# Optimization experiments

Measured on AMD Instinct MI355X. Metric: run time of the kernel, lower is better.

## Reference

```python
import jax, jax.numpy as jnp
import numpy as np


def setup_inputs() -> dict:
    key = jax.random.key(0)
    kq, kk, kv = jax.random.split(key, 3)
    B, S, H, D = 1, 4096, 16, 64
    q = jax.random.normal(kq, (B, S, H, D), dtype=jnp.float32)
    k = jax.random.normal(kk, (B, S, H, D), dtype=jnp.float32)
    v = jax.random.normal(kv, (B, S, H, D), dtype=jnp.float32)
    return {"q": q, "k": k, "v": v, "causal": 1}


def reference(q, k, v, causal):
    B, S, H, D = q.shape
    scale = D ** (-0.5)
    # scores: [B, H, S_q, S_k]
    scores = jnp.einsum("bqhd,bkhd->bhqk", q, k) * scale
    if causal:
        mask = jnp.triu(jnp.ones((S, S), dtype=bool), k=1)  # True above diagonal
        scores = jnp.where(mask, -jnp.inf, scores)
    attn = jax.nn.softmax(scores, axis=-1)
    out = jnp.einsum("bhqk,bkhd->bqhd", attn, v)
    return out
```

## Files before the change

### kernel.cpp

```cpp
#include <hip/hip_runtime.h>
#include <stdint.h>

#define S_LEN 4096
#define NH    16
#define HD    64
#define RSTR  (NH * HD)
#define LRSTR 18

typedef __attribute__((ext_vector_type(8))) __bf16 bf16x8;
typedef __attribute__((ext_vector_type(4))) short short4v;
typedef __attribute__((ext_vector_type(4))) float floatx4;

union BF4 { unsigned short u[4]; unsigned d[2]; short4v s; };

__device__ __forceinline__ unsigned pkbf(float a, float b) {
    unsigned ua = __builtin_bit_cast(unsigned, a) + 0x8000u;
    unsigned ub = __builtin_bit_cast(unsigned, b) + 0x8000u;
    return __builtin_amdgcn_perm(ub, ua, 0x07060302u);
}

__device__ __forceinline__ floatx4 mfma16(short4v a, short4v b, floatx4 c) {
#if __has_builtin(__builtin_amdgcn_mfma_f32_16x16x16bf16_1k)
    return __builtin_amdgcn_mfma_f32_16x16x16bf16_1k(a, b, c, 0, 0, 0);
#else
    floatx4 d;
    asm volatile("v_mfma_f32_16x16x16_bf16 %0, %1, %2, %3\n\ts_nop 7\n\ts_nop 7"
                 : "=v"(d) : "v"(a), "v"(b), "v"(c));
    return d;
#endif
}

__device__ __forceinline__ void gl16(const void* g, void* l) {
#if __has_builtin(__builtin_amdgcn_global_load_lds)
    __builtin_amdgcn_global_load_lds((const __attribute__((address_space(1))) unsigned int*)g,
                                     (__attribute__((address_space(3))) unsigned int*)l, 16, 0, 0);
#else
    *(uint4*)l = *(const uint4*)g;
#endif
}

__global__ __launch_bounds__(256)
void pp_kv(const float* __restrict__ K, const float* __restrict__ V,
           unsigned short* __restrict__ Kz, unsigned short* __restrict__ Vz) {
    __shared__ __align__(16) float vt[64][68];
    const int bid = blockIdx.x;
    const int h   = bid & 15;
    const int tau = bid >> 4;
    const int tid = threadIdx.x;
    {
        const int r = tid >> 2, gg = tid & 3;
        const float* kp = K + ((size_t)(64 * tau + r) * NH + h) * HD + 16 * gg;
        const float4 a = *reinterpret_cast<const float4*>(kp);
        const float4 b = *reinterpret_cast<const float4*>(kp + 4);
        const float4 c = *reinterpret_cast<const float4*>(kp + 8);
        const float4 d = *reinterpret_cast<const float4*>(kp + 12);
        uint4 f0, f1;
        f0.x = pkbf(a.x, a.y); f0.y = pkbf(a.z, a.w);
        f0.z = pkbf(b.x, b.y); f0.w = pkbf(b.z, b.w);
        f1.x = pkbf(c.x, c.y); f1.y = pkbf(c.z, c.w);
        f1.z = pkbf(d.x, d.y); f1.w = pkbf(d.z, d.w);
        unsigned short* out = Kz + ((size_t)(h * 64 + tau)) * 4096 + r * 64;
        *reinterpret_cast<uint4*>(out + (((2 * gg)     ^ (r & 7)) * 8)) = f0;
        *reinterpret_cast<uint4*>(out + (((2 * gg + 1) ^ (r & 7)) * 8)) = f1;
    }
    {
        const int r = tid >> 2, ch = tid & 3;
        const float* vrow = V + ((size_t)(64 * tau + r) * NH + h) * HD + 4 * ch;
        #pragma unroll
        for (int k2 = 0; k2 < 4; ++k2)
            *reinterpret_cast<float4*>(&vt[r][4 * ch + 16 * k2]) =
                *reinterpret_cast<const float4*>(vrow + 16 * k2);
    }
    __syncthreads();
    {
        const int dr = tid & 63, kg = tid >> 6;
        float x[16];
        #pragma unroll
        for (int j = 0; j < 16; ++j) x[j] = vt[16 * kg + j][dr];
        uint4 g0, g1;
        g0.x = pkbf(x[0],  x[1]);  g0.y = pkbf(x[2],  x[3]);
        g0.z = pkbf(x[4],  x[5]);  g0.w = pkbf(x[6],  x[7]);
        g1.x = pkbf(x[8],  x[9]);  g1.y = pkbf(x[10], x[11]);
        g1.z = pkbf(x[12], x[13]); g1.w = pkbf(x[14], x[15]);
        unsigned short* out = Vz + ((size_t)(h * 64 + tau)) * 4096 + dr * 64;
        *reinterpret_cast<uint4*>(out + (((2 * kg)     ^ (dr & 7)) * 8)) = g0;
        *reinterpret_cast<uint4*>(out + (((2 * kg + 1) ^ (dr & 7)) * 8)) = g1;
    }
}

__global__ __launch_bounds__(256, 3)
void fa_main(const float* __restrict__ Q, const unsigned short* __restrict__ Kz,
             const unsigned short* __restrict__ Vz, const int* __restrict__ causal_p,
             float* __restrict__ O) {
    __shared__ __align__(16) unsigned char smem[49152];
    unsigned short* Klds = (unsigned short*)smem;
    unsigned short* Vlds = (unsigned short*)(smem + 24576);
    unsigned short* Qlds = (unsigned short*)(smem + 16384);
    float* Lsum = (float*)smem;
    float* Lred = (float*)(smem + 16384);

    const int bid = blockIdx.x;
    const int h   = bid & 15;
    const int x   = 63 - (bid >> 4);
    const int q0  = x * 64;

    const int tid = threadIdx.x;
    const int wv  = tid >> 6;
    const int ln  = tid & 63;
    const int c16 = ln & 15;
    const int qd  = ln >> 4;
    const int causal = causal_p[0];

    const float SC = 0.18033688011112042f;

    const char* kg = (const char*)Kz + (size_t)h * 64 * 8192 + wv * 2048 + ln * 16;
    const char* vg = (const char*)Vz + (size_t)h * 64 * 8192 + wv * 2048 + ln * 16;
    char* kl = (char*)smem + wv * 2048 + ln * 16;
    char* vl = (char*)smem + 24576 + wv * 2048 + ln * 16;

#define GLDS_TILE(IT, BUF) do {                                  \
    const char* ks_ = kg + (size_t)(IT) * 8192;                  \
    const char* vs_ = vg + (size_t)(IT) * 8192;                  \
    char* kd_ = kl + (BUF) * 8192;                               \
    char* vd_ = vl + (BUF) * 8192;                               \
    gl16(ks_, kd_); gl16(ks_ + 1024, kd_ + 1024);                \
    gl16(vs_, vd_); gl16(vs_ + 1024, vd_ + 1024);                \
} while (0)

    GLDS_TILE(0, 0);
    GLDS_TILE(1, 1);

    {
        const int r = tid >> 2, gg = tid & 3;
        const float* qp = Q + ((size_t)(q0 + r) * NH + h) * HD + 16 * gg;
        const float4 a = *reinterpret_cast<const float4*>(qp);
        const float4 b = *reinterpret_cast<const float4*>(qp + 4);
        const float4 c = *reinterpret_cast<const float4*>(qp + 8);
        const float4 d = *reinterpret_cast<const float4*>(qp + 12);
        uint4 f0, f1;
        f0.x = pkbf(a.x * SC, a.y * SC); f0.y = pkbf(a.z * SC, a.w * SC);
        f0.z = pkbf(b.x * SC, b.y * SC); f0.w = pkbf(b.z * SC, b.w * SC);
        f1.x = pkbf(c.x * SC, c.y * SC); f1.y = pkbf(c.z * SC, c.w * SC);
        f1.z = pkbf(d.x * SC, d.y * SC); f1.w = pkbf(d.z * SC, d.w * SC);
        unsigned short* out = Qlds + r * 64;
        *reinterpret_cast<uint4*>(out + (((2 * gg)     ^ (r & 7)) * 8)) = f0;
        *reinterpret_cast<uint4*>(out + (((2 * gg + 1) ^ (r & 7)) * 8)) = f1;
    }

    const int nIter = causal ? (x + 1) : (S_LEN / 64);

    floatx4 acc[4][4];
    #pragma unroll
    for (int m = 0; m < 4; ++m)
        #pragma unroll
        for (int t = 0; t < 4; ++t) acc[m][t] = floatx4{0.f, 0.f, 0.f, 0.f};
    float lacc[4] = {0.f, 0.f, 0.f, 0.f};

    const int e7 = c16 & 7;
    const int o0 = (qd ^ e7) * 8;
    const int o1 = ((4 + qd) ^ e7) * 8;
    const int vo = ((2 * wv + (qd >> 1)) ^ e7) * 8 + (qd & 1) * 4;
    const int mlhs = 16 * wv + 4 * qd;

    __syncthreads();

    bf16x8 qh0[4], qh1[4];
    #pragma unroll
    for (int t = 0; t < 4; ++t) {
        const unsigned short* qrow = Qlds + (16 * t + c16) * 64;
        qh0[t] = *reinterpret_cast<const bf16x8*>(qrow + o0);
        qh1[t] = *reinterpret_cast<const bf16x8*>(qrow + o1);
    }
    __syncthreads();

    int br = 0;
    int b2 = 2;
    for (int it = 0; it < nIter; ++it) {
        if (it == nIter - 1) {
            asm volatile("s_waitcnt vmcnt(0)" ::: "memory");
        } else {
            asm volatile("s_waitcnt vmcnt(4)" ::: "memory");
        }
        __builtin_amdgcn_s_barrier();

        if (it + 2 < nIter) GLDS_TILE(it + 2, b2);

        const unsigned short* Kb = Klds + br * 4096;
        const unsigned short* Vb = Vlds + br * 4096;

        const unsigned short* krow = Kb + (16 * wv + c16) * 64;
        const bf16x8 kf0 = *reinterpret_cast<const bf16x8*>(krow + o0);
        const bf16x8 kf1 = *reinterpret_cast<const bf16x8*>(krow + o1);

        const bool maskit = (causal != 0) && (it == nIter - 1);

        BF4 pf[4];
        #pragma unroll
        for (int t = 0; t < 4; ++t) {
            floatx4 st = __builtin_amdgcn_mfma_f32_16x16x32_bf16(
                kf0, qh0[t], floatx4{0.f, 0.f, 0.f, 0.f}, 0, 0, 0);
            st = __builtin_amdgcn_mfma_f32_16x16x32_bf16(kf1, qh1[t], st, 0, 0, 0);
            float p[4];
            #pragma unroll
            for (int i = 0; i < 4; ++i) {
                float sv = st[i];
                if (maskit && (mlhs + i > 16 * t + c16)) sv = -1e30f;
                p[i] = __builtin_amdgcn_exp2f(sv);
            }
            lacc[t] += (p[0] + p[1]) + (p[2] + p[3]);
            pf[t].d[0] = pkbf(p[0], p[1]);
            pf[t].d[1] = pkbf(p[2], p[3]);
        }

        #pragma unroll
        for (int md = 0; md < 4; ++md) {
            BF4 vf;
            const unsigned short* vrow = Vb + (16 * md + c16) * 64 + vo;
            *reinterpret_cast<uint2*>(&vf.d[0]) = *reinterpret_cast<const uint2*>(vrow);
            #pragma unroll
            for (int t = 0; t < 4; ++t)
                acc[md][t] = mfma16(vf.s, pf[t].s, acc[md][t]);
        }

        br = (br == 2) ? 0 : br + 1;
        b2 = (b2 == 2) ? 0 : b2 + 1;
    }

    __syncthreads();

    #pragma unroll
    for (int t = 0; t < 4; ++t) {
        float lt = lacc[t];
        lt += __shfl_xor(lt, 16);
        lt += __shfl_xor(lt, 32);
        if (qd == 0) Lsum[wv * 64 + t * 16 + c16] = lt;
    }

    const int qi  = tid & 63;
    const int dg  = tid >> 6;
    const int lnr = 16 * dg + (qi & 15);
    const int jb  = 4 * (qi >> 4);
    float* orow = O + ((size_t)(q0 + qi) * NH + h) * HD;
    float inv = 0.f;

    for (int md = 0; md < 4; ++md) {
        float* Lw = Lred + (wv * 64 + ln) * LRSTR;
        #pragma unroll
        for (int t = 0; t < 4; ++t) {
            float2 w0; w0.x = acc[md][t][0]; w0.y = acc[md][t][1];
            float2 w1; w1.x = acc[md][t][2]; w1.y = acc[md][t][3];
            *reinterpret_cast<float2*>(&Lw[4 * t])     = w0;
            *reinterpret_cast<float2*>(&Lw[4 * t + 2]) = w1;
        }
        __syncthreads();
        if (md == 0) {
            const float l = Lsum[qi] + Lsum[64 + qi] + Lsum[128 + qi] + Lsum[192 + qi];
            inv = 1.0f / l;
        }
        float s0 = 0.f, s1 = 0.f, s2 = 0.f, s3 = 0.f;
        #pragma unroll
        for (int w = 0; w < 4; ++w) {
            const float* Lr = Lred + (w * 64 + lnr) * LRSTR + jb;
            s0 += Lr[0]; s1 += Lr[1]; s2 += Lr[2]; s3 += Lr[3];
        }
        floatx4 o; o[0] = s0 * inv; o[1] = s1 * inv; o[2] = s2 * inv; o[3] = s3 * inv;
        *reinterpret_cast<floatx4*>(orow + 16 * md + 4 * dg) = o;
        __syncthreads();
    }
}

extern "C" void kernel_launch(void* const* d_in, const int* in_sizes, int n_in,
                              void* d_out, int out_size, void* d_ws, size_t ws_size,
                              hipStream_t stream) {
    const float* q = (const float*)d_in[0];
    const float* k = (const float*)d_in[1];
    const float* v = (const float*)d_in[2];
    const int* causal = (const int*)d_in[3];
    float* out = (float*)d_out;
    unsigned short* Kz = (unsigned short*)d_ws;
    unsigned short* Vz = Kz + (size_t)NH * 64 * 4096;
    pp_kv<<<dim3(64 * NH), dim3(256), 0, stream>>>(k, v, Kz, Vz);
    fa_main<<<dim3(64 * NH), dim3(256), 0, stream>>>(q, Kz, Vz, causal, out);
}
```

Baseline: 142.3 us.

## Software-pipeline QK^T scores one tile ahead of softmax and PV

Computes the score MFMAs for the first K tile before the loop, and in each iteration computes the next tile's scores after the PV MFMAs. This lets exp2 and packing overlap with independent MFMA work. To do this the K tile for iteration it+1 must already be in LDS, so the vmcnt wait tightens from 4 to 2. The stricter wait may reduce load/compute overlap, and the extra live score registers add register pressure.

After: 144.6 us. No clear change (+1.6%).

```diff
diff --git a/kernel.cpp b/kernel.cpp
--- a/kernel.cpp
+++ b/kernel.cpp
@@ -173,37 +173,50 @@
     }
     __syncthreads();
 
+    floatx4 stc[4];
+    {
+        const unsigned short* krow = Klds + (16 * wv + c16) * 64;
+        const bf16x8 kf0 = *reinterpret_cast<const bf16x8*>(krow + o0);
+        const bf16x8 kf1 = *reinterpret_cast<const bf16x8*>(krow + o1);
+        #pragma unroll
+        for (int t = 0; t < 4; ++t) {
+            floatx4 st = __builtin_amdgcn_mfma_f32_16x16x32_bf16(
+                kf0, qh0[t], floatx4{0.f, 0.f, 0.f, 0.f}, 0, 0, 0);
+            stc[t] = __builtin_amdgcn_mfma_f32_16x16x32_bf16(kf1, qh1[t], st, 0, 0, 0);
+        }
+    }
+
     int br = 0;
+    int b1 = 1;
     int b2 = 2;
     for (int it = 0; it < nIter; ++it) {
         if (it == nIter - 1) {
             asm volatile("s_waitcnt vmcnt(0)" ::: "memory");
         } else {
-            asm volatile("s_waitcnt vmcnt(4)" ::: "memory");
+            asm volatile("s_waitcnt vmcnt(2)" ::: "memory");
         }
         __builtin_amdgcn_s_barrier();
 
         if (it + 2 < nIter) GLDS_TILE(it + 2, b2);
 
-        const unsigned short* Kb = Klds + br * 4096;
-        const unsigned short* Vb = Vlds + br * 4096;
-
-        const unsigned short* krow = Kb + (16 * wv + c16) * 64;
-        const bf16x8 kf0 = *reinterpret_cast<const bf16x8*>(krow + o0);
-        const bf16x8 kf1 = *reinterpret_cast<const bf16x8*>(krow + o1);
+        const bool have_next = (it + 1 < nIter);
+
+        bf16x8 nkf0, nkf1;
+        if (have_next) {
+            const unsigned short* krow = Klds + b1 * 4096 + (16 * wv + c16) * 64;
+            nkf0 = *reinterpret_cast<const bf16x8*>(krow + o0);
+            nkf1 = *reinterpret_cast<const bf16x8*>(krow + o1);
+        }
 
         const bool maskit = (causal != 0) && (it == nIter - 1);
 
         BF4 pf[4];
         #pragma unroll
         for (int t = 0; t < 4; ++t) {
-            floatx4 st = __builtin_amdgcn_mfma_f32_16x16x32_bf16(
-                kf0, qh0[t], floatx4{0.f, 0.f, 0.f, 0.f}, 0, 0, 0);
-            st = __builtin_amdgcn_mfma_f32_16x16x32_bf16(kf1, qh1[t], st, 0, 0, 0);
             float p[4];
             #pragma unroll
             for (int i = 0; i < 4; ++i) {
-                float sv = st[i];
+                float sv = stc[t][i];
                 if (maskit && (mlhs + i > 16 * t + c16)) sv = -1e30f;
                 p[i] = __builtin_amdgcn_exp2f(sv);
             }
@@ -212,6 +225,7 @@
             pf[t].d[1] = pkbf(p[2], p[3]);
         }
 
+        const unsigned short* Vb = Vlds + br * 4096;
         #pragma unroll
         for (int md = 0; md < 4; ++md) {
             BF4 vf;
@@ -222,8 +236,16 @@
                 acc[md][t] = mfma16(vf.s, pf[t].s, acc[md][t]);
         }
 
-        br = (br == 2) ? 0 : br + 1;
-        b2 = (b2 == 2) ? 0 : b2 + 1;
+        if (have_next) {
+            #pragma unroll
+            for (int t = 0; t < 4; ++t) {
+                floatx4 st = __builtin_amdgcn_mfma_f32_16x16x32_bf16(
+                    nkf0, qh0[t], floatx4{0.f, 0.f, 0.f, 0.f}, 0, 0, 0);
+                stc[t] = __builtin_amdgcn_mfma_f32_16x16x32_bf16(nkf1, qh1[t], st, 0, 0, 0);
+            }
+        }
+
+        const int t0 = br; br = b1; b1 = b2; b2 = t0;
     }
 
     __syncthreads();
```
